# Kernel tuning notes

Measured on AMD Instinct MI355X. Metric: run time of the kernel, lower is better.

## Reference

```python
import jax, jax.numpy as jnp
import numpy as np

T, S, B = 128, 128, 32          # enc len, dec len, batch
H, D = 512, 512                 # hidden == input_size (required by module)
VE, VD = 32000, 32000           # encoder / decoder vocab


def setup_inputs() -> dict:
    key = jax.random.key(0)
    ks = jax.random.split(key, 14)
    s = 0.05  # init scale, mimics uniform(-initrange, initrange)
    n = lambda k, shape: jax.random.normal(k, shape, dtype=jnp.float32) * s
    return {
        "encoder_inputs": jax.random.randint(ks[0], (T, B), 0, VE),
        "decoder_inputs": jax.random.randint(ks[1], (S, B), 0, VD),
        "enc_emb": n(ks[2], (VE, D)),
        "dec_emb": n(ks[3], (VD, D)),
        "enc_Wih": n(ks[4], (4 * H, D)),   # torch LSTM gate order: i,f,g,o
        "enc_Whh": n(ks[5], (4 * H, H)),
        "dec_Wih": n(ks[6], (4 * H, H)),
        "dec_Whh": n(ks[7], (4 * H, H)),
        "attn_enc_W": n(ks[8], (H, H)),
        "attn_enc_b": n(ks[9], (H,)),
        "attn_dec_W": n(ks[10], (H, H)),
        "attn_dec_b": n(ks[11], (H,)),
        "out_W": n(ks[12], (VD, H)),
        "out_b": n(ks[13], (VD,)),
    }


def lstm(x, Wih, Whh, h0, c0):
    """Bias-free LSTM over seq-first x [T,B,Din]; returns (ys [T,B,H], (h,c))."""
    def step(carry, xt):
        h, c = carry
        gates = xt @ Wih.T + h @ Whh.T
        i, f, g, o = jnp.split(gates, 4, axis=-1)
        c = jax.nn.sigmoid(f) * c + jax.nn.sigmoid(i) * jnp.tanh(g)
        h = jax.nn.sigmoid(o) * jnp.tanh(c)
        return (h, c), h
    (h, c), ys = jax.lax.scan(step, (h0, c0), x)
    return ys, (h, c)


def reference(encoder_inputs, decoder_inputs, enc_emb, dec_emb,
              enc_Wih, enc_Whh, dec_Wih, dec_Whh,
              attn_enc_W, attn_enc_b, attn_dec_W, attn_dec_b,
              out_W, out_b):
    Bsz = encoder_inputs.shape[1]
    Hd = enc_Whh.shape[1]
    z = jnp.zeros((Bsz, Hd), dtype=enc_Whh.dtype)
    # encoder
    xe = enc_emb[encoder_inputs]                      # [T,B,D]
    enc_out, (h, c) = lstm(xe, enc_Wih, enc_Whh, z, z)
    # decoder (teacher forcing), init from encoder final state
    xd = dec_emb[decoder_inputs]                      # [S,B,H]
    dec_out, _ = lstm(xd, dec_Wih, dec_Whh, h, c)     # [S,B,H]
    # per-timestep dot attention, vectorized over all decoder steps
    scores = jnp.einsum('tbh,sbh->sbt', enc_out, dec_out)   # [S,B,T]
    attn = jax.nn.softmax(scores, axis=-1)
    ctx = jnp.einsum('sbt,tbh->sbh', attn, enc_out)          # [S,B,H]
    hidden = jnp.tanh(ctx @ attn_enc_W.T + attn_enc_b
                      + dec_out @ attn_dec_W.T + attn_dec_b)
    logits = hidden @ out_W.T + out_b                        # [S,B,VD]
    return jax.nn.log_softmax(logits, axis=-1)
```

## Files before the change

kernel.cpp:

```cpp
#include <hip/hip_runtime.h>
#include <stdint.h>

#define TT 128
#define BB 32
#define HH 512
#define MM 4096
#define VD 32000
#define NLB 16

typedef float f32x4 __attribute__((ext_vector_type(4)));
typedef float f32x2 __attribute__((ext_vector_type(2)));
typedef short s16x8 __attribute__((ext_vector_type(8)));
typedef unsigned long long u64;

#define TAGMASK 0x0001000100010001ull

__device__ __forceinline__ ushort f2bf(float f){
  uint u = __float_as_uint(f);
  return (ushort)((u + 0x7fffu + ((u >> 16) & 1u)) >> 16);
}
__device__ __forceinline__ float bfl(uint v){ return __uint_as_float(v << 16); }
__device__ __forceinline__ float bfh(uint v){ return __uint_as_float(v & 0xffff0000u); }
__device__ __forceinline__ float fast_tanh(float x){
  return 1.f - 2.f / (1.f + __expf(2.f * x));
}
__device__ __forceinline__ float sigm(float x){ return 1.f / (1.f + __expf(-x)); }

__global__ void k_init(u64* hbuf){
  int i = blockIdx.x * 256 + threadIdx.x;
  if (i < 4096) hbuf[i] = 0ull;
  else if (i < 8192) hbuf[i] = TAGMASK;
}

__global__ __launch_bounds__(256) void k_cvt(const float* __restrict__ s, ushort* __restrict__ d, int n4){
  int i = blockIdx.x * 256 + threadIdx.x;
  int st = gridDim.x * 256;
  for (; i < n4; i += st){
    f32x4 v = *(const f32x4*)(s + (size_t)i * 4);
    ushort4 o; o.x = f2bf(v[0]); o.y = f2bf(v[1]); o.z = f2bf(v[2]); o.w = f2bf(v[3]);
    *(ushort4*)(d + (size_t)i * 4) = o;
  }
}

__global__ __launch_bounds__(128) void k_embed(const int* __restrict__ ids, const float* __restrict__ emb,
                                               ushort* __restrict__ out){
  int row = blockIdx.x, t = threadIdx.x;
  int id = ids[row];
  f32x4 v = *(const f32x4*)(emb + (size_t)id * HH + t * 4);
  ushort4 o; o.x = f2bf(v[0]); o.y = f2bf(v[1]); o.z = f2bf(v[2]); o.w = f2bf(v[3]);
  *(ushort4*)(out + (size_t)row * HH + t * 4) = o;
}

__global__ __launch_bounds__(128) void k_concatB(const float* __restrict__ We, const float* __restrict__ Wd,
                                                 ushort* __restrict__ Bc){
  int n = blockIdx.x, t = threadIdx.x;
  f32x4 a = *(const f32x4*)(We + (size_t)n * HH + t * 4);
  f32x4 b = *(const f32x4*)(Wd + (size_t)n * HH + t * 4);
  ushort4 oa, ob;
  oa.x = f2bf(a[0]); oa.y = f2bf(a[1]); oa.z = f2bf(a[2]); oa.w = f2bf(a[3]);
  ob.x = f2bf(b[0]); ob.y = f2bf(b[1]); ob.z = f2bf(b[2]); ob.w = f2bf(b[3]);
  *(ushort4*)(Bc + (size_t)n * 1024 + t * 4) = oa;
  *(ushort4*)(Bc + (size_t)n * 1024 + 512 + t * 4) = ob;
}
__global__ void k_bsum(const float* a, const float* b, float* o){
  int i = blockIdx.x * 256 + threadIdx.x;
  if (i < HH) o[i] = a[i] + b[i];
}

template<bool BIAS, bool TANH, bool OUTBF, bool LSE>
__global__ __launch_bounds__(256) void k_gemm(const ushort* __restrict__ A, const ushort* __restrict__ Bm,
                                              const float* __restrict__ bias, void* __restrict__ Cout,
                                              int Mtot, int Ntot, int K,
                                              float* __restrict__ pbufM, float* __restrict__ pbufL){
  __shared__ __align__(16) ushort As[128 * 32];
  __shared__ __align__(16) ushort Bs[128 * 32];
  __shared__ float sMm[2][128], sMl[2][128];
  const int tid = threadIdx.x;
  const int m0 = blockIdx.y << 7, n0 = blockIdx.x << 7;
  const int wid = tid >> 6, lane = tid & 63;
  const int wm = wid >> 1, wn = wid & 1;
  const int lr = lane & 15, lg = lane >> 4;
  const int lk = lg << 3, cr = lg << 2;
  f32x4 acc[4][4];
  for (int i = 0; i < 4; ++i)
    for (int j = 0; j < 4; ++j)
      acc[i][j] = (f32x4){0.f, 0.f, 0.f, 0.f};
  const int c0 = tid, c1 = tid + 256;
  const size_t ar0 = (size_t)(m0 + (c0 >> 2)) * K + ((c0 & 3) << 3);
  const size_t ar1 = (size_t)(m0 + (c1 >> 2)) * K + ((c1 & 3) << 3);
  const size_t br0 = (size_t)(n0 + (c0 >> 2)) * K + ((c0 & 3) << 3);
  const size_t br1 = (size_t)(n0 + (c1 >> 2)) * K + ((c1 & 3) << 3);
  for (int k0 = 0; k0 < K; k0 += 32){
    __syncthreads();
    __builtin_amdgcn_global_load_lds((const __attribute__((address_space(1))) void*)(A + ar0 + k0),
                                     (__attribute__((address_space(3))) void*)(As + (c0 << 3)), 16, 0, 0);
    __builtin_amdgcn_global_load_lds((const __attribute__((address_space(1))) void*)(A + ar1 + k0),
                                     (__attribute__((address_space(3))) void*)(As + (c1 << 3)), 16, 0, 0);
    __builtin_amdgcn_global_load_lds((const __attribute__((address_space(1))) void*)(Bm + br0 + k0),
                                     (__attribute__((address_space(3))) void*)(Bs + (c0 << 3)), 16, 0, 0);
    __builtin_amdgcn_global_load_lds((const __attribute__((address_space(1))) void*)(Bm + br1 + k0),
                                     (__attribute__((address_space(3))) void*)(Bs + (c1 << 3)), 16, 0, 0);
    __syncthreads();
    s16x8 af[4], bf[4];
    #pragma unroll
    for (int f = 0; f < 4; ++f){
      af[f] = *(const s16x8*)(As + ((wm << 6) + (f << 4) + lr) * 32 + lk);
      bf[f] = *(const s16x8*)(Bs + ((wn << 6) + (f << 4) + lr) * 32 + lk);
    }
    #pragma unroll
    for (int fm = 0; fm < 4; ++fm)
      #pragma unroll
      for (int fn = 0; fn < 4; ++fn)
        acc[fm][fn] = __builtin_amdgcn_mfma_f32_16x16x32_bf16(af[fm], bf[fn], acc[fm][fn], 0, 0, 0);
  }
  float bv4[4];
  #pragma unroll
  for (int fn = 0; fn < 4; ++fn)
    bv4[fn] = BIAS ? bias[n0 + (wn << 6) + (fn << 4) + lr] : 0.f;
  float mv[16], lv[16];
  #pragma unroll
  for (int fm = 0; fm < 4; ++fm){
    #pragma unroll
    for (int r = 0; r < 4; ++r){
      const int rw = m0 + (wm << 6) + (fm << 4) + cr + r;
      float vs[4], vmax = -1e30f;
      #pragma unroll
      for (int fn = 0; fn < 4; ++fn){
        float v = acc[fm][fn][r] + bv4[fn];
        if (TANH) v = tanhf(v);
        vs[fn] = v;
        if (LSE) vmax = fmaxf(vmax, v);
        const size_t off = (size_t)rw * Ntot + (n0 + (wn << 6) + (fn << 4) + lr);
        if (OUTBF) ((ushort*)Cout)[off] = f2bf(v);
        else       ((float*)Cout)[off] = v;
      }
      if (LSE){
        float l4 = 0.f;
        #pragma unroll
        for (int fn = 0; fn < 4; ++fn) l4 += __expf(vs[fn] - vmax);
        mv[(fm << 2) + r] = vmax; lv[(fm << 2) + r] = l4;
      }
    }
  }
  if (LSE){
    #pragma unroll
    for (int q = 0; q < 16; ++q){
      #pragma unroll
      for (int off = 1; off < 16; off <<= 1){
        float m2 = __shfl_xor(mv[q], off), l2 = __shfl_xor(lv[q], off);
        float nm = fmaxf(mv[q], m2);
        lv[q] = lv[q] * __expf(mv[q] - nm) + l2 * __expf(m2 - nm);
        mv[q] = nm;
      }
    }
    float selM = -1e30f, selL = 0.f;
    #pragma unroll
    for (int q = 0; q < 16; ++q){
      selM = (lr == q) ? mv[q] : selM;
      selL = (lr == q) ? lv[q] : selL;
    }
    const int lrow = (wm << 6) + ((lr >> 2) << 4) + (lg << 2) + (lr & 3);
    sMm[wn][lrow] = selM; sMl[wn][lrow] = selL;
    __syncthreads();
    if (tid < 128){
      float ma = sMm[0][tid], mb = sMm[1][tid];
      float nm = fmaxf(ma, mb);
      float l = sMl[0][tid] * __expf(ma - nm) + sMl[1][tid] * __expf(mb - nm);
      pbufM[(size_t)(m0 + tid) * 256 + blockIdx.x] = nm;
      pbufL[(size_t)(m0 + tid) * 256 + blockIdx.x] = l;
    }
  }
}

__global__ __launch_bounds__(512) void k_lstm(const float* __restrict__ GinE, const float* __restrict__ GinD,
                                              const float* __restrict__ WhhE, const float* __restrict__ WhhD,
                                              u64* __restrict__ hbuf,
                                              ushort* __restrict__ encO, ushort* __restrict__ decO,
                                              ushort* __restrict__ Ac){
  __shared__ __align__(16) ushort wlds[4 * 32 * 512];
  __shared__ __align__(16) uint4 abuf[2048];
  const int tid = threadIdx.x;
  const int bk = blockIdx.x;
  const int J0 = bk << 5;
  const int w = tid >> 6, lane = tid & 63;
  const int m = w & 1, jt = w >> 1;
  const int lr = lane & 15, lg = lane >> 4;
  const int beta = lane >> 2, p = lane & 3, myr = beta & 3;
  const int b_own = (m << 4) + beta;
  const int j_own = J0 + (jt << 3) + (p << 1);

  float cc0 = 0.f, cc1 = 0.f;
  const int sgb = (lane & 48) + ((lane & 3) << 1);
  const int ad_l0 = sgb << 2, ad_l1 = (sgb + 1) << 2;
  const int ad_h0 = (sgb + 8) << 2, ad_h1 = (sgb + 9) << 2;
  const char* wrow0 = (const char*)wlds + ((((lr >> 3) << 5) + (jt << 3) + (lr & 7)) << 10);
  const char* wrow1 = wrow0 + (64 << 10);
  const int swz = (lr & 7) << 4;

  auto stageW = [&](const float* Whh){
    const int rr = tid >> 2, kq = tid & 3;
    const int gg = rr >> 5, jl = rr & 31;
    const float* src = Whh + (size_t)((gg << 9) + J0 + jl) * 512 + (kq << 7);
    char* dstrow = (char*)wlds + (size_t)(((gg << 5) + jl) << 10);
    #pragma unroll
    for (int i = 0; i < 16; ++i){
      f32x4 wa = *(const f32x4*)(src + (i << 3));
      f32x4 wc = *(const f32x4*)(src + (i << 3) + 4);
      uint4 pk;
      pk.x = ((uint)f2bf(wa[1]) << 16) | f2bf(wa[0]);
      pk.y = ((uint)f2bf(wa[3]) << 16) | f2bf(wa[2]);
      pk.z = ((uint)f2bf(wc[1]) << 16) | f2bf(wc[0]);
      pk.w = ((uint)f2bf(wc[3]) << 16) | f2bf(wc[2]);
      *(uint4*)(dstrow + ((((kq << 4) + i) << 4) ^ ((jl & 7) << 4))) = pk;
    }
  };

  float gi0, gi1, gf0, gf1, gg0, gg1, go0, go1;
  f32x2 nxi, nxf, nxg, nxo;
  {
    const float* gp = GinE + (size_t)b_own * 2048 + j_own;
    nxi = *(const f32x2*)(gp);        nxf = *(const f32x2*)(gp + 512);
    nxg = *(const f32x2*)(gp + 1024); nxo = *(const f32x2*)(gp + 1536);
  }
  stageW(WhhE);
  { uint4 z = {0u, 0u, 0u, 0u};
    #pragma unroll
    for (int i = 0; i < 4; ++i) abuf[(tid << 2) + i] = z; }
  __syncthreads();

  for (int s = 0; s < 256; ++s){
    const int ph = s >> 7, t = s & 127;
    if (s == 128){ stageW(WhhD); __syncthreads(); }
    gi0 = nxi[0]; gi1 = nxi[1]; gf0 = nxf[0]; gf1 = nxf[1];
    gg0 = nxg[0]; gg1 = nxg[1]; go0 = nxo[0]; go1 = nxo[1];
    if (s < 255){
      const int s2 = s + 1, t2 = s2 & 127;
      const float* G2 = (s2 >> 7) ? GinD : GinE;
      const float* gp = G2 + (size_t)((t2 << 5) + b_own) * 2048 + j_own;
      nxi = *(const f32x2*)(gp);        nxf = *(const f32x2*)(gp + 512);
      nxg = *(const f32x2*)(gp + 1024); nxo = *(const f32x2*)(gp + 1536);
    }
    f32x4 a0 = {0.f, 0.f, 0.f, 0.f}, a1 = {0.f, 0.f, 0.f, 0.f};
    #pragma unroll
    for (int ks = 0; ks < 16; ++ks){
      union { uint4 u; s16x8 v; } ua;
      ua.u = abuf[(m << 10) + (ks << 6) + (lg << 4) + lr];
      const int ko = ((ks << 6) + (lg << 4)) ^ swz;
      const s16x8 b0 = *(const s16x8*)(wrow0 + ko);
      const s16x8 b1 = *(const s16x8*)(wrow1 + ko);
      a0 = __builtin_amdgcn_mfma_f32_16x16x32_bf16(ua.v, b0, a0, 0, 0, 0);
      a1 = __builtin_amdgcn_mfma_f32_16x16x32_bf16(ua.v, b1, a1, 0, 0, 0);
    }
    float vi0 = 0.f, vi1 = 0.f, vf0 = 0.f, vf1 = 0.f, vg0 = 0.f, vg1 = 0.f, vo0 = 0.f, vo1 = 0.f;
    #pragma unroll
    for (int r = 0; r < 4; ++r){
      const int ti0 = __builtin_amdgcn_ds_bpermute(ad_l0, __float_as_int(a0[r]));
      const int ti1 = __builtin_amdgcn_ds_bpermute(ad_l1, __float_as_int(a0[r]));
      const int tf0 = __builtin_amdgcn_ds_bpermute(ad_h0, __float_as_int(a0[r]));
      const int tf1 = __builtin_amdgcn_ds_bpermute(ad_h1, __float_as_int(a0[r]));
      const int tg0 = __builtin_amdgcn_ds_bpermute(ad_l0, __float_as_int(a1[r]));
      const int tg1 = __builtin_amdgcn_ds_bpermute(ad_l1, __float_as_int(a1[r]));
      const int to0 = __builtin_amdgcn_ds_bpermute(ad_h0, __float_as_int(a1[r]));
      const int to1 = __builtin_amdgcn_ds_bpermute(ad_h1, __float_as_int(a1[r]));
      if (myr == r){
        vi0 = __int_as_float(ti0); vi1 = __int_as_float(ti1);
        vf0 = __int_as_float(tf0); vf1 = __int_as_float(tf1);
        vg0 = __int_as_float(tg0); vg1 = __int_as_float(tg1);
        vo0 = __int_as_float(to0); vo1 = __int_as_float(to1);
      }
    }
    const uint tgn = (uint)(((s + 1) >> 1) & 1);
    float h0f, h1f;
    { const float si = sigm(vi0 + gi0), sf = sigm(vf0 + gf0), so = sigm(vo0 + go0);
      cc0 = sf * cc0 + si * fast_tanh(vg0 + gg0); h0f = so * fast_tanh(cc0); }
    { const float si = sigm(vi1 + gi1), sf = sigm(vf1 + gf1), so = sigm(vo1 + go1);
      cc1 = sf * cc1 + si * fast_tanh(vg1 + gg1); h1f = so * fast_tanh(cc1); }
    const uint hb0 = (uint)f2bf(h0f), hb1 = (uint)f2bf(h1f);
    const uint hclean = (hb1 << 16) | hb0;
    const uint htag = (((hb1 & 0xFFFEu) | tgn) << 16) | ((hb0 & 0xFFFEu) | tgn);
    __hip_atomic_store((uint*)hbuf + (((s + 1) & 1) << 13) + (m << 12) + (bk << 8) + (jt << 6) + (beta << 2) + p,
                       htag, __ATOMIC_RELAXED, __HIP_MEMORY_SCOPE_AGENT);
    uint* hall = (uint*)(ph ? decO : encO);
    hall[((size_t)((t << 5) + b_own) << 8) + (j_own >> 1)] = hclean;
    if (ph) ((uint*)Ac)[((size_t)((t << 5) + b_own) << 9) + 256 + (j_own >> 1)] = hclean;
    if (w >= 6 && s < 255){
      const uint pat = (((s + 1) >> 1) & 1) ? 0x00010001u : 0u;
      const char* hp = (const char*)hbuf + (((s + 1) & 1) << 15) + (m << 14) + (lg << 8) + (lr << 4);
      uint4 vv[16];
      for (;;){
        #pragma unroll
        for (int ks = 0; ks < 16; ++ks)
          asm volatile("global_load_dwordx4 %0, %1, off sc0 sc1"
                       : "=v"(vv[ks]) : "v"(hp + (ks << 10)) : "memory");
        asm volatile("s_waitcnt vmcnt(0)" ::: "memory");
        __builtin_amdgcn_sched_barrier(0);
        uint bad = 0u;
        #pragma unroll
        for (int ks = 0; ks < 16; ++ks)
          bad |= (vv[ks].x ^ pat) | (vv[ks].y ^ pat) | (vv[ks].z ^ pat) | (vv[ks].w ^ pat);
        if (__all((bad & 0x00010001u) == 0u)) break;
      }
      char* ab = (char*)abuf + (m << 14) + (lg << 8) + (lr << 4);
      #pragma unroll
      for (int ks = 0; ks < 16; ++ks){
        vv[ks].x &= 0xFFFEFFFEu; vv[ks].y &= 0xFFFEFFFEu;
        vv[ks].z &= 0xFFFEFFFEu; vv[ks].w &= 0xFFFEFFFEu;
        *(uint4*)(ab + (ks << 10)) = vv[ks];
      }
    }
    __syncthreads();
  }
}

__global__ __launch_bounds__(256) void k_attn(const ushort* __restrict__ enc, const ushort* __restrict__ dec,
                                              ushort* __restrict__ Ac){
  __shared__ __align__(16) float dec_lds[16 * 512];
  __shared__ __align__(16) float P[16 * 128];
  const int tid = threadIdx.x;
  const int b = blockIdx.x & 31, st = blockIdx.x >> 5;
  const int s0 = st << 4;
  for (int j = 0; j < 4; ++j){
    int e8 = tid + (j << 8);
    int sl = e8 >> 6, k = (e8 & 63) << 3;
    uint4 v = *(const uint4*)(dec + ((size_t)((s0 + sl) * 32 + b) << 9) + k);
    float* dst = dec_lds + sl * 512 + k;
    dst[0] = bfl(v.x); dst[1] = bfh(v.x); dst[2] = bfl(v.y); dst[3] = bfh(v.y);
    dst[4] = bfl(v.z); dst[5] = bfh(v.z); dst[6] = bfl(v.w); dst[7] = bfh(v.w);
  }
  __syncthreads();
  {
    const int tl = tid & 127, sh = tid >> 7;
    const ushort* erow = enc + ((size_t)(tl * 32 + b) << 9);
    float acc8[8] = {0.f, 0.f, 0.f, 0.f, 0.f, 0.f, 0.f, 0.f};
    for (int k = 0; k < 512; k += 8){
      uint4 v = *(const uint4*)(erow + k);
      const float e0 = bfl(v.x), e1 = bfh(v.x), e2 = bfl(v.y), e3 = bfh(v.y);
      const float e4 = bfl(v.z), e5 = bfh(v.z), e6 = bfl(v.w), e7 = bfh(v.w);
      const float* dl = dec_lds + (sh << 3) * 512 + k;
      #pragma unroll
      for (int i = 0; i < 8; ++i){
        f32x4 d0 = *(const f32x4*)(dl + i * 512);
        f32x4 d1 = *(const f32x4*)(dl + i * 512 + 4);
        acc8[i] += d0[0]*e0 + d0[1]*e1 + d0[2]*e2 + d0[3]*e3
                 + d1[0]*e4 + d1[1]*e5 + d1[2]*e6 + d1[3]*e7;
      }
    }
    #pragma unroll
    for (int i = 0; i < 8; ++i) P[((sh << 3) + i) * 128 + tl] = acc8[i];
  }
  __syncthreads();
  {
    const int r = tid >> 4, i = tid & 15;
    float* prow = P + r * 128 + (i << 3);
    float v[8], mx = -1e30f;
    #pragma unroll
    for (int j = 0; j < 8; ++j){ v[j] = prow[j]; mx = fmaxf(mx, v[j]); }
    #pragma unroll
    for (int off = 1; off < 16; off <<= 1) mx = fmaxf(mx, __shfl_xor(mx, off));
    float l = 0.f;
    #pragma unroll
    for (int j = 0; j < 8; ++j){ v[j] = __expf(v[j] - mx); l += v[j]; }
    #pragma unroll
    for (int off = 1; off < 16; off <<= 1) l += __shfl_xor(l, off);
    const float inv = 1.f / l;
    #pragma unroll
    for (int j = 0; j < 8; ++j) prow[j] = v[j] * inv;
  }
  __syncthreads();
  {
    const int h0 = tid << 1;
    float acc[16][2];
    #pragma unroll
    for (int sl = 0; sl < 16; ++sl){ acc[sl][0] = 0.f; acc[sl][1] = 0.f; }
    const ushort* ecol = enc + ((size_t)b << 9) + h0;
    for (int t = 0; t < 128; ++t){
      uint v = *(const uint*)(ecol + (size_t)t * 16384);
      const float e0 = bfl(v), e1 = bfh(v);
      #pragma unroll
      for (int sl = 0; sl < 16; ++sl){
        const float p = P[sl * 128 + t];
        acc[sl][0] += p * e0; acc[sl][1] += p * e1;
      }
    }
    #pragma unroll
    for (int sl = 0; sl < 16; ++sl){
      const int mm = (s0 + sl) * 32 + b;
      uint u = ((uint)f2bf(acc[sl][1]) << 16) | (uint)f2bf(acc[sl][0]);
      *(uint*)(Ac + (size_t)mm * 1024 + h0) = u;
    }
  }
}

__global__ __launch_bounds__(256) void k_sub(float* __restrict__ out,
                                             const float* __restrict__ pM, const float* __restrict__ pL){
  __shared__ float slse;
  const int row = blockIdx.x;
  const int tid = threadIdx.x;
  if (tid < 64){
    float m = -1e30f, l = 0.f;
    for (int i = tid; i < 250; i += 64){
      float m2 = pM[(size_t)row * 256 + i], l2 = pL[(size_t)row * 256 + i];
      float nm = fmaxf(m, m2);
      l = l * __expf(m - nm) + l2 * __expf(m2 - nm);
      m = nm;
    }
    #pragma unroll
    for (int off = 32; off; off >>= 1){
      float m2 = __shfl_xor(m, off), l2 = __shfl_xor(l, off);
      float nm = fmaxf(m, m2);
      l = l * __expf(m - nm) + l2 * __expf(m2 - nm);
      m = nm;
    }
    if (tid == 0) slse = m + __logf(l);
  }
  __syncthreads();
  const float s = slse;
  float* p = out + (size_t)row * VD;
  for (int i4 = tid; i4 < VD / 4; i4 += 256){
    f32x4 v = *(const f32x4*)(p + ((size_t)i4 << 2));
    v[0] -= s; v[1] -= s; v[2] -= s; v[3] -= s;
    *(f32x4*)(p + ((size_t)i4 << 2)) = v;
  }
}

extern "C" void kernel_launch(void* const* d_in, const int* in_sizes, int n_in,
                              void* d_out, int out_size, void* d_ws, size_t ws_size,
                              hipStream_t stream){
  const int*   enc_in  = (const int*)d_in[0];
  const int*   dec_in  = (const int*)d_in[1];
  const float* enc_emb = (const float*)d_in[2];
  const float* dec_emb = (const float*)d_in[3];
  const float* WihE    = (const float*)d_in[4];
  const float* WhhE    = (const float*)d_in[5];
  const float* WihD    = (const float*)d_in[6];
  const float* WhhD    = (const float*)d_in[7];
  const float* We      = (const float*)d_in[8];
  const float* be      = (const float*)d_in[9];
  const float* Wd      = (const float*)d_in[10];
  const float* bd      = (const float*)d_in[11];
  const float* outW    = (const float*)d_in[12];
  const float* outb    = (const float*)d_in[13];
  float* out = (float*)d_out;

  char* ws = (char*)d_ws;
  size_t off = 0;
  auto alloc = [&](size_t bytes){ void* p = ws + off; off += (bytes + 255) & ~(size_t)255; return p; };
  ushort* xe    = (ushort*)alloc((size_t)MM * HH * 2);
  ushort* xd    = (ushort*)alloc((size_t)MM * HH * 2);
  ushort* WihEb = (ushort*)alloc((size_t)2048 * 512 * 2);
  ushort* WihDb = (ushort*)alloc((size_t)2048 * 512 * 2);
  ushort* Bc    = (ushort*)alloc((size_t)512 * 1024 * 2);
  float*  bsum  = (float*)alloc(512 * 4);
  ushort* outWb = (ushort*)alloc((size_t)VD * HH * 2);
  ushort* encO  = (ushort*)alloc((size_t)MM * HH * 2);
  ushort* decO  = (ushort*)alloc((size_t)MM * HH * 2);
  u64*    hbuf  = (u64*)alloc(8192 * 8);
  ushort* Ac    = (ushort*)alloc((size_t)MM * 1024 * 2);
  ushort* hid   = (ushort*)alloc((size_t)MM * HH * 2);
  float*  pbufM = (float*)alloc((size_t)MM * 256 * 4);
  float*  pbufL = (float*)alloc((size_t)MM * 256 * 4);
  float* GinE = out;
  float* GinD = out + (size_t)MM * 2048;

  k_init<<<dim3(32), dim3(256), 0, stream>>>(hbuf);
  k_cvt<<<dim3(1024), dim3(256), 0, stream>>>(WihE, WihEb, 2048 * 512 / 4);
  k_cvt<<<dim3(1024), dim3(256), 0, stream>>>(WihD, WihDb, 2048 * 512 / 4);
  k_cvt<<<dim3(2048), dim3(256), 0, stream>>>(outW, outWb, VD * HH / 4);
  k_concatB<<<dim3(512), dim3(128), 0, stream>>>(We, Wd, Bc);
  k_bsum<<<dim3(2), dim3(256), 0, stream>>>(be, bd, bsum);
  k_embed<<<dim3(MM), dim3(128), 0, stream>>>(enc_in, enc_emb, xe);
  k_embed<<<dim3(MM), dim3(128), 0, stream>>>(dec_in, dec_emb, xd);
  k_gemm<false, false, false, false><<<dim3(16, 32), dim3(256), 0, stream>>>(xe, WihEb, (const float*)nullptr, GinE, MM, 2048, 512, nullptr, nullptr);
  k_gemm<false, false, false, false><<<dim3(16, 32), dim3(256), 0, stream>>>(xd, WihDb, (const float*)nullptr, GinD, MM, 2048, 512, nullptr, nullptr);
  k_lstm<<<dim3(NLB), dim3(512), 0, stream>>>(GinE, GinD, WhhE, WhhD, hbuf, encO, decO, Ac);
  k_attn<<<dim3(256), dim3(256), 0, stream>>>(encO, decO, Ac);
  k_gemm<true, true, true, false><<<dim3(4, 32), dim3(256), 0, stream>>>(Ac, Bc, bsum, hid, MM, 512, 1024, nullptr, nullptr);
  k_gemm<true, false, false, true><<<dim3(250, 32), dim3(256), 0, stream>>>(hid, outWb, outb, out, MM, VD, 512, pbufM, pbufL);
  k_sub<<<dim3(MM), dim3(256), 0, stream>>>(out, pbufM, pbufL);
}
```

Measured before the change: 1.709 ms.

## Have every LSTM wave poll hidden state directly, removing per-step LDS staging and barrier

Before, two waves per block spun on the global tagged hidden-state buffer, copied the new h into an LDS buffer, and then the whole block synchronised before the next step's MFMA. Now each wave polls the global buffer itself at the start of every step and feeds the loaded, tag-masked values straight into the MFMAs. This removes the LDS round trip and the per-step block barrier; a barrier is kept only around the decoder weight restage. The MFMA accumulation is also split into two independent chains per output to shorten the dependency chain. In exchange, all eight waves now issue coherent global polling loads, which raises L2 traffic, and correctness at step 0 relies on the hidden-state buffer starting at zero.

```diff
diff --git a/kernel.cpp b/kernel.cpp
--- a/kernel.cpp
+++ b/kernel.cpp
@@ -178,7 +178,6 @@
                                               ushort* __restrict__ encO, ushort* __restrict__ decO,
                                               ushort* __restrict__ Ac){
   __shared__ __align__(16) ushort wlds[4 * 32 * 512];
-  __shared__ __align__(16) uint4 abuf[2048];
   const int tid = threadIdx.x;
   const int bk = blockIdx.x;
   const int J0 = bk << 5;
@@ -215,24 +214,38 @@
     }
   };
 
-  float gi0, gi1, gf0, gf1, gg0, gg1, go0, go1;
   f32x2 nxi, nxf, nxg, nxo;
-  {
-    const float* gp = GinE + (size_t)b_own * 2048 + j_own;
+  { const float* gp = GinE + (size_t)b_own * 2048 + j_own;
     nxi = *(const f32x2*)(gp);        nxf = *(const f32x2*)(gp + 512);
-    nxg = *(const f32x2*)(gp + 1024); nxo = *(const f32x2*)(gp + 1536);
-  }
+    nxg = *(const f32x2*)(gp + 1024); nxo = *(const f32x2*)(gp + 1536); }
   stageW(WhhE);
-  { uint4 z = {0u, 0u, 0u, 0u};
-    #pragma unroll
-    for (int i = 0; i < 4; ++i) abuf[(tid << 2) + i] = z; }
   __syncthreads();
 
   for (int s = 0; s < 256; ++s){
     const int ph = s >> 7, t = s & 127;
-    if (s == 128){ stageW(WhhD); __syncthreads(); }
-    gi0 = nxi[0]; gi1 = nxi[1]; gf0 = nxf[0]; gf1 = nxf[1];
-    gg0 = nxg[0]; gg1 = nxg[1]; go0 = nxo[0]; go1 = nxo[1];
+    if (s == 128){
+      __syncthreads();
+      stageW(WhhD);
+      __syncthreads();
+    }
+    const uint pat = ((s >> 1) & 1) ? 0x00010001u : 0u;
+    const char* hp = (const char*)hbuf + ((s & 1) << 15) + (m << 14) + (lg << 8) + (lr << 4);
+    uint4 vv[16];
+    for (;;){
+      #pragma unroll
+      for (int ks = 0; ks < 16; ++ks)
+        asm volatile("global_load_dwordx4 %0, %1, off sc0 sc1"
+                     : "=v"(vv[ks]) : "v"(hp + (ks << 10)) : "memory");
+      asm volatile("s_waitcnt vmcnt(0)" ::: "memory");
+      __builtin_amdgcn_sched_barrier(0);
+      uint bad = 0u;
+      #pragma unroll
+      for (int ks = 0; ks < 16; ++ks)
+        bad |= (vv[ks].x ^ pat) | (vv[ks].y ^ pat) | (vv[ks].z ^ pat) | (vv[ks].w ^ pat);
+      if (__all((bad & 0x00010001u) == 0u)) break;
+    }
+    const float gi0 = nxi[0], gi1 = nxi[1], gf0 = nxf[0], gf1 = nxf[1];
+    const float gg0 = nxg[0], gg1 = nxg[1], go0 = nxo[0], go1 = nxo[1];
     if (s < 255){
       const int s2 = s + 1, t2 = s2 & 127;
       const float* G2 = (s2 >> 7) ? GinD : GinE;
@@ -240,17 +253,27 @@
       nxi = *(const f32x2*)(gp);        nxf = *(const f32x2*)(gp + 512);
       nxg = *(const f32x2*)(gp + 1024); nxo = *(const f32x2*)(gp + 1536);
     }
-    f32x4 a0 = {0.f, 0.f, 0.f, 0.f}, a1 = {0.f, 0.f, 0.f, 0.f};
+    f32x4 a0 = {0.f, 0.f, 0.f, 0.f}, a0b = {0.f, 0.f, 0.f, 0.f};
+    f32x4 a1 = {0.f, 0.f, 0.f, 0.f}, a1b = {0.f, 0.f, 0.f, 0.f};
     #pragma unroll
     for (int ks = 0; ks < 16; ++ks){
       union { uint4 u; s16x8 v; } ua;
-      ua.u = abuf[(m << 10) + (ks << 6) + (lg << 4) + lr];
+      ua.u.x = vv[ks].x & 0xFFFEFFFEu;
+      ua.u.y = vv[ks].y & 0xFFFEFFFEu;
+      ua.u.z = vv[ks].z & 0xFFFEFFFEu;
+      ua.u.w = vv[ks].w & 0xFFFEFFFEu;
       const int ko = ((ks << 6) + (lg << 4)) ^ swz;
       const s16x8 b0 = *(const s16x8*)(wrow0 + ko);
       const s16x8 b1 = *(const s16x8*)(wrow1 + ko);
-      a0 = __builtin_amdgcn_mfma_f32_16x16x32_bf16(ua.v, b0, a0, 0, 0, 0);
-      a1 = __builtin_amdgcn_mfma_f32_16x16x32_bf16(ua.v, b1, a1, 0, 0, 0);
-    }
+      if (ks & 1){
+        a0b = __builtin_amdgcn_mfma_f32_16x16x32_bf16(ua.v, b0, a0b, 0, 0, 0);
+        a1b = __builtin_amdgcn_mfma_f32_16x16x32_bf16(ua.v, b1, a1b, 0, 0, 0);
+      } else {
+        a0 = __builtin_amdgcn_mfma_f32_16x16x32_bf16(ua.v, b0, a0, 0, 0, 0);
+        a1 = __builtin_amdgcn_mfma_f32_16x16x32_bf16(ua.v, b1, a1, 0, 0, 0);
+      }
+    }
+    a0 += a0b; a1 += a1b;
     float vi0 = 0.f, vi1 = 0.f, vf0 = 0.f, vf1 = 0.f, vg0 = 0.f, vg1 = 0.f, vo0 = 0.f, vo1 = 0.f;
     #pragma unroll
     for (int r = 0; r < 4; ++r){
@@ -283,32 +306,6 @@
     uint* hall = (uint*)(ph ? decO : encO);
     hall[((size_t)((t << 5) + b_own) << 8) + (j_own >> 1)] = hclean;
     if (ph) ((uint*)Ac)[((size_t)((t << 5) + b_own) << 9) + 256 + (j_own >> 1)] = hclean;
-    if (w >= 6 && s < 255){
-      const uint pat = (((s + 1) >> 1) & 1) ? 0x00010001u : 0u;
-      const char* hp = (const char*)hbuf + (((s + 1) & 1) << 15) + (m << 14) + (lg << 8) + (lr << 4);
-      uint4 vv[16];
-      for (;;){
-        #pragma unroll
-        for (int ks = 0; ks < 16; ++ks)
-          asm volatile("global_load_dwordx4 %0, %1, off sc0 sc1"
-                       : "=v"(vv[ks]) : "v"(hp + (ks << 10)) : "memory");
-        asm volatile("s_waitcnt vmcnt(0)" ::: "memory");
-        __builtin_amdgcn_sched_barrier(0);
-        uint bad = 0u;
-        #pragma unroll
-        for (int ks = 0; ks < 16; ++ks)
-          bad |= (vv[ks].x ^ pat) | (vv[ks].y ^ pat) | (vv[ks].z ^ pat) | (vv[ks].w ^ pat);
-        if (__all((bad & 0x00010001u) == 0u)) break;
-      }
-      char* ab = (char*)abuf + (m << 14) + (lg << 8) + (lr << 4);
-      #pragma unroll
-      for (int ks = 0; ks < 16; ++ks){
-        vv[ks].x &= 0xFFFEFFFEu; vv[ks].y &= 0xFFFEFFFEu;
-        vv[ks].z &= 0xFFFEFFFEu; vv[ks].w &= 0xFFFEFFFEu;
-        *(uint4*)(ab + (ks << 10)) = vv[ks];
-      }
-    }
-    __syncthreads();
   }
 }
 
```

Result: slower. 1.978 ms (+15.8%).
